# Optimization experiments

Hardware: AMD Instinct MI355X
Metric: run time of the kernel (lower is better)

Reference implementation:

```python
import jax, jax.numpy as jnp
import numpy as np

B, S, D = 2, 4096, 1024
H = 16
HD = D // H  # head_dim = 64

def setup_inputs() -> dict:
    key = jax.random.key(0)
    ks = jax.random.split(key, 9)
    sc = 1.0 / np.sqrt(D)
    return {
        "X":   jax.random.normal(ks[0], (B, S, D), dtype=jnp.float32),
        "Wq":  jax.random.normal(ks[1], (D, D), dtype=jnp.float32) * sc,
        "bq":  jax.random.normal(ks[2], (D,), dtype=jnp.float32) * 0.01,
        "Wk":  jax.random.normal(ks[3], (D, D), dtype=jnp.float32) * sc,
        "bk":  jax.random.normal(ks[4], (D,), dtype=jnp.float32) * 0.01,
        "Wv":  jax.random.normal(ks[5], (D, D), dtype=jnp.float32) * sc,
        "bv":  jax.random.normal(ks[6], (D,), dtype=jnp.float32) * 0.01,
        "Wo":  jax.random.normal(ks[7], (D, D), dtype=jnp.float32) * sc,
        "bo":  jax.random.normal(ks[8], (D,), dtype=jnp.float32) * 0.01,
    }

def reference(X, Wq, bq, Wk, bk, Wv, bv, Wo, bo):
    b, s, d = X.shape
    h, hd = H, HD
    # projections
    Q = X @ Wq + bq
    K = X @ Wk + bk
    V = X @ Wv + bv
    # [b, h, s, hd]
    Q = Q.reshape(b, s, h, hd).transpose(0, 2, 1, 3)
    K = K.reshape(b, s, h, hd).transpose(0, 2, 1, 3)
    V = V.reshape(b, s, h, hd).transpose(0, 2, 1, 3)
    scale = 1.0 / jnp.sqrt(jnp.asarray(hd, dtype=X.dtype))  # sqrt(hidden/num_heads)
    scores = jnp.einsum("bhqd,bhkd->bhqk", Q, K) * scale
    attn = jax.nn.softmax(scores, axis=-1)
    out = jnp.einsum("bhqk,bhkd->bhqd", attn, V)
    out = out.transpose(0, 2, 1, 3).reshape(b, s, d)
    return out @ Wo + bo
```

## Files before the change

kernel.cpp:

```cpp
#include <hip/hip_runtime.h>

#define Bsz 2
#define Sq  4096
#define Dm  1024
#define NH  16
#define HD  64

typedef __attribute__((ext_vector_type(8))) short short8;
typedef __attribute__((ext_vector_type(4))) float f32x4;
typedef __attribute__((ext_vector_type(2))) __fp16 fp16x2;
typedef __attribute__((ext_vector_type(4))) _Float16 half4v;

__device__ __forceinline__ unsigned short f2bf(float x) {
    unsigned int u = __float_as_uint(x);
    u += 0x7fffu + ((u >> 16) & 1u);
    return (unsigned short)(u >> 16);
}

__device__ __forceinline__ void gl2lds16(const unsigned short* g, unsigned short* l) {
    __builtin_amdgcn_global_load_lds(
        (const __attribute__((address_space(1))) unsigned int*)g,
        (__attribute__((address_space(3))) unsigned int*)l, 16, 0, 0);
}

__global__ __launch_bounds__(256) void cvt_bf16(const float4* __restrict__ in,
                                                ushort4* __restrict__ out) {
    const int i = blockIdx.x * 256 + threadIdx.x;
    const float4 v = in[i];
    ushort4 r;
    r.x = f2bf(v.x); r.y = f2bf(v.y); r.z = f2bf(v.z); r.w = f2bf(v.w);
    out[i] = r;
}

__global__ __launch_bounds__(256) void wtrans(const float* __restrict__ W,
                                              unsigned short* __restrict__ Wt) {
    __shared__ float tile[64][65];
    const int k0 = blockIdx.y * 64, n0 = blockIdx.x * 64;
    const int t = threadIdx.x;
    #pragma unroll
    for (int i = 0; i < 16; ++i) {
        const int idx = t + i * 256, r = idx >> 6, c = idx & 63;
        tile[r][c] = W[(size_t)(k0 + r) * Dm + n0 + c];
    }
    __syncthreads();
    #pragma unroll
    for (int i = 0; i < 16; ++i) {
        const int idx = t + i * 256, rr = idx >> 6, cc = idx & 63;
        Wt[(size_t)(n0 + rr) * Dm + k0 + cc] = f2bf(tile[cc][rr]);
    }
}

template <int MODE>
__global__ __launch_bounds__(256) void gemm_mfma(
    const unsigned short* __restrict__ A,
    const unsigned short* __restrict__ Bt,
    const float* __restrict__ bias,
    void* __restrict__ Cout, float oscale)
{
    __shared__ unsigned short As[128 * 32];
    __shared__ unsigned short Bs[128 * 32];

    const int bm = blockIdx.y * 128;
    const int bn = blockIdx.x * 128;
    const int t    = threadIdx.x;
    const int w    = t >> 6;
    const int lane = t & 63;
    const int quad = lane >> 4;
    const int c16  = lane & 15;
    const int wm = (w >> 1) * 64;
    const int wn = (w & 1) * 64;

    f32x4 acc[4][4];
    #pragma unroll
    for (int i = 0; i < 4; ++i)
        #pragma unroll
        for (int j = 0; j < 4; ++j)
            acc[i][j] = (f32x4){0.f, 0.f, 0.f, 0.f};

    const int srow = lane >> 2, soff = (lane & 3) * 8;
    const unsigned short* Ag0 = A  + (size_t)(bm + w * 16 + srow) * Dm + soff;
    const unsigned short* Ag1 = Ag0 + (size_t)64 * Dm;
    const unsigned short* Bg0 = Bt + (size_t)(bn + w * 16 + srow) * Dm + soff;
    const unsigned short* Bg1 = Bg0 + (size_t)64 * Dm;
    unsigned short* Al0 = As + (w * 16) * 32;
    unsigned short* Al1 = As + (64 + w * 16) * 32;
    unsigned short* Bl0 = Bs + (w * 16) * 32;
    unsigned short* Bl1 = Bs + (64 + w * 16) * 32;

    for (int k0 = 0; k0 < Dm; k0 += 32) {
        __syncthreads();
        gl2lds16(Ag0 + k0, Al0);
        gl2lds16(Ag1 + k0, Al1);
        gl2lds16(Bg0 + k0, Bl0);
        gl2lds16(Bg1 + k0, Bl1);
        __syncthreads();

        short8 af[4], bf[4];
        #pragma unroll
        for (int mt = 0; mt < 4; ++mt)
            af[mt] = *(const short8*)(As + (wm + mt * 16 + c16) * 32 + quad * 8);
        #pragma unroll
        for (int nt = 0; nt < 4; ++nt)
            bf[nt] = *(const short8*)(Bs + (wn + nt * 16 + c16) * 32 + quad * 8);
        #pragma unroll
        for (int mt = 0; mt < 4; ++mt)
            #pragma unroll
            for (int nt = 0; nt < 4; ++nt)
                acc[mt][nt] = __builtin_amdgcn_mfma_f32_16x16x32_bf16(
                    af[mt], bf[nt], acc[mt][nt], 0, 0, 0);
    }

    #pragma unroll
    for (int mt = 0; mt < 4; ++mt) {
        const int m0 = bm + wm + mt * 16 + quad * 4;
        #pragma unroll
        for (int nt = 0; nt < 4; ++nt) {
            const int n = bn + wn + nt * 16 + c16;
            const float bv = bias[n];
            if (MODE == 0) {
                float* C = (float*)Cout;
                #pragma unroll
                for (int r = 0; r < 4; ++r)
                    C[(size_t)(m0 + r) * Dm + n] = acc[mt][nt][r] + bv;
            } else if (MODE == 1) {
                unsigned short* C = (unsigned short*)Cout;
                const int h = n >> 6, d = n & 63;
                #pragma unroll
                for (int r = 0; r < 4; ++r) {
                    const int m = m0 + r;
                    const int b = m >> 12, s = m & (Sq - 1);
                    C[((size_t)(b * NH + h) * Sq + s) * HD + d] =
                        f2bf((acc[mt][nt][r] + bv) * oscale);
                }
            } else {
                unsigned short* C = (unsigned short*)Cout;
                const int h = n >> 6, d = n & 63;
                const int b = m0 >> 12, s0 = m0 & (Sq - 1);
                union { fp16x2 h2[2]; unsigned int u[2]; } pk;
                pk.h2[0] = __builtin_amdgcn_cvt_pkrtz(acc[mt][nt][0] + bv,
                                                      acc[mt][nt][1] + bv);
                pk.h2[1] = __builtin_amdgcn_cvt_pkrtz(acc[mt][nt][2] + bv,
                                                      acc[mt][nt][3] + bv);
                *(uint2*)(C + ((size_t)(b * NH + h) * HD + d) * Sq + s0) =
                    make_uint2(pk.u[0], pk.u[1]);
            }
        }
    }
}

__global__ __launch_bounds__(256, 2) void attn_mfma3(
    const unsigned short* __restrict__ Q,
    const unsigned short* __restrict__ K,
    const unsigned short* __restrict__ Vt,
    unsigned short* __restrict__ AO)
{
    __shared__ unsigned short Ks[2][64 * 72];
    __shared__ unsigned short Vs[2][64 * 72];

    const int qt = blockIdx.x;
    const int bh = blockIdx.y;
    const int b = bh >> 4, h = bh & 15;
    const int t    = threadIdx.x;
    const int w    = t >> 6;
    const int lane = t & 63;
    const int quad = lane >> 4;
    const int c16  = lane & 15;
    const size_t base = (size_t)bh * Sq * HD;

    short8 qf[4][2];
    #pragma unroll
    for (int qg = 0; qg < 4; ++qg) {
        const unsigned short* qp =
            Q + base + (size_t)(qt * 256 + w * 64 + qg * 16 + c16) * HD;
        qf[qg][0] = *(const short8*)(qp + quad * 8);
        qf[qg][1] = *(const short8*)(qp + 32 + quad * 8);
    }

    f32x4 O[4][4];
    f32x4 Lsum[4];
    #pragma unroll
    for (int qg = 0; qg < 4; ++qg) {
        Lsum[qg] = (f32x4){0.f, 0.f, 0.f, 0.f};
        #pragma unroll
        for (int g = 0; g < 4; ++g)
            O[qg][g] = (f32x4){0.f, 0.f, 0.f, 0.f};
    }
    const half4v ones = {(_Float16)1.f, (_Float16)1.f, (_Float16)1.f, (_Float16)1.f};

    const int srow = t >> 2, sc4 = (t & 3) * 8;
    const unsigned short* kg = K  + base + (size_t)srow * HD + sc4;
    const unsigned short* vg = Vt + base + (size_t)srow * Sq + sc4;
    unsigned short* ksl = &Ks[0][0] + srow * 72 + sc4;
    unsigned short* vsl = &Vs[0][0] + srow * 72 + sc4;
    const int LBUF = 64 * 72;

    int4 kr0, kr1, vr0, vr1;
    kr0 = *(const int4*)(kg);
    kr1 = *(const int4*)(kg + 32);
    vr0 = *(const int4*)(vg);
    vr1 = *(const int4*)(vg + 32);
    *(int4*)(ksl)      = kr0;
    *(int4*)(ksl + 32) = kr1;
    *(int4*)(vsl)      = vr0;
    *(int4*)(vsl + 32) = vr1;

    for (int kt = 0; kt < Sq / 64; ++kt) {
        const int cur = kt & 1;
        if (kt + 1 < Sq / 64) {
            const unsigned short* kp = kg + (size_t)(kt + 1) * 64 * HD;
            const unsigned short* vp = vg + (kt + 1) * 64;
            kr0 = *(const int4*)(kp);
            kr1 = *(const int4*)(kp + 32);
            vr0 = *(const int4*)(vp);
            vr1 = *(const int4*)(vp + 32);
        }
        __syncthreads();

        const unsigned short* ksb = &Ks[cur][0];
        const unsigned short* vsb = &Vs[cur][0];

        half4v Pfrag[4][4];
        #pragma unroll
        for (int nt = 0; nt < 4; ++nt) {
            const int krow = nt * 16 + c16;
            const short8 kf0 = *(const short8*)(ksb + krow * 72 + quad * 8);
            const short8 kf1 = *(const short8*)(ksb + krow * 72 + 32 + quad * 8);
            #pragma unroll
            for (int qg = 0; qg < 4; ++qg) {
                f32x4 z = (f32x4){0.f, 0.f, 0.f, 0.f};
                z = __builtin_amdgcn_mfma_f32_16x16x32_bf16(kf0, qf[qg][0], z, 0, 0, 0);
                z = __builtin_amdgcn_mfma_f32_16x16x32_bf16(kf1, qf[qg][1], z, 0, 0, 0);
                const float p0 = __builtin_amdgcn_exp2f(z[0]);
                const float p1 = __builtin_amdgcn_exp2f(z[1]);
                const float p2 = __builtin_amdgcn_exp2f(z[2]);
                const float p3 = __builtin_amdgcn_exp2f(z[3]);
                union { fp16x2 h2[2]; half4v h4; } pk;
                pk.h2[0] = __builtin_amdgcn_cvt_pkrtz(p0, p1);
                pk.h2[1] = __builtin_amdgcn_cvt_pkrtz(p2, p3);
                Pfrag[qg][nt] = pk.h4;
            }
        }

        #pragma unroll
        for (int kk = 0; kk < 4; ++kk) {
            #pragma unroll
            for (int g = 0; g < 4; ++g) {
                const half4v vf = *(const half4v*)
                    (vsb + (g * 16 + c16) * 72 + kk * 16 + quad * 4);
                #pragma unroll
                for (int qg = 0; qg < 4; ++qg)
                    O[qg][g] = __builtin_amdgcn_mfma_f32_16x16x16f16(
                        Pfrag[qg][kk], vf, O[qg][g], 0, 0, 0);
            }
            #pragma unroll
            for (int qg = 0; qg < 4; ++qg)
                Lsum[qg] = __builtin_amdgcn_mfma_f32_16x16x16f16(
                    Pfrag[qg][kk], ones, Lsum[qg], 0, 0, 0);
        }

        if (kt + 1 < Sq / 64) {
            const int nb = cur ^ 1;
            *(int4*)(ksl + nb * LBUF)      = kr0;
            *(int4*)(ksl + nb * LBUF + 32) = kr1;
            *(int4*)(vsl + nb * LBUF)      = vr0;
            *(int4*)(vsl + nb * LBUF + 32) = vr1;
        }
    }

    #pragma unroll
    for (int qg = 0; qg < 4; ++qg) {
        float linv[4];
        #pragma unroll
        for (int r = 0; r < 4; ++r) linv[r] = 1.f / Lsum[qg][r];
        #pragma unroll
        for (int g = 0; g < 4; ++g) {
            const int col = h * HD + g * 16 + c16;
            #pragma unroll
            for (int r = 0; r < 4; ++r) {
                const int s = qt * 256 + w * 64 + qg * 16 + quad * 4 + r;
                AO[((size_t)(b * Sq + s)) * Dm + col] = f2bf(O[qg][g][r] * linv[r]);
            }
        }
    }
}

extern "C" void kernel_launch(void* const* d_in, const int* in_sizes, int n_in,
                              void* d_out, int out_size, void* d_ws, size_t ws_size,
                              hipStream_t stream)
{
    const float* X  = (const float*)d_in[0];
    const float* Wq = (const float*)d_in[1];
    const float* bq = (const float*)d_in[2];
    const float* Wk = (const float*)d_in[3];
    const float* bk = (const float*)d_in[4];
    const float* Wv = (const float*)d_in[5];
    const float* bv = (const float*)d_in[6];
    const float* Wo = (const float*)d_in[7];
    const float* bo = (const float*)d_in[8];
    float* out = (float*)d_out;

    unsigned short* ws = (unsigned short*)d_ws;
    const size_t NX = (size_t)Bsz * Sq * Dm;
    const size_t NW = (size_t)Dm * Dm;
    unsigned short* Xb  = ws; ws += NX;
    unsigned short* Wtq = ws; ws += NW;
    unsigned short* Wtk = ws; ws += NW;
    unsigned short* Wtv = ws; ws += NW;
    unsigned short* Wto = ws; ws += NW;
    unsigned short* Qh  = ws; ws += NX;
    unsigned short* Kh  = ws; ws += NX;
    unsigned short* Vt  = ws; ws += NX;
    unsigned short* AO  = ws; ws += NX;

    cvt_bf16<<<(int)(NX / 1024), 256, 0, stream>>>((const float4*)X, (ushort4*)Xb);
    dim3 tg(16, 16);
    wtrans<<<tg, 256, 0, stream>>>(Wq, Wtq);
    wtrans<<<tg, 256, 0, stream>>>(Wk, Wtk);
    wtrans<<<tg, 256, 0, stream>>>(Wv, Wtv);
    wtrans<<<tg, 256, 0, stream>>>(Wo, Wto);

    const float SCL = 0.18033688011112042f;
    dim3 gg(Dm / 128, (Bsz * Sq) / 128);
    gemm_mfma<1><<<gg, 256, 0, stream>>>(Xb, Wtq, bq, Qh, SCL);
    gemm_mfma<1><<<gg, 256, 0, stream>>>(Xb, Wtk, bk, Kh, 1.0f);
    gemm_mfma<2><<<gg, 256, 0, stream>>>(Xb, Wtv, bv, Vt, 1.0f);

    attn_mfma3<<<dim3(Sq / 256, Bsz * NH), 256, 0, stream>>>(Qh, Kh, Vt, AO);

    gemm_mfma<0><<<gg, 256, 0, stream>>>(AO, Wto, bo, out, 1.0f);
}
```

Before: 389.2 us.

## Merge QKV GEMMs and weight transposes, halve attention query tile

Merges the four weight-transpose launches into one 3D-grid launch. The three Q/K/V projection GEMMs become a single launch over a concatenated weight buffer, with the output mode chosen per block. The attention kernel now handles 128 queries per block instead of 256, which doubles the grid to 1024 blocks, and raises the launch-bounds occupancy hint to 4 blocks. This targets launch overhead and under-filled grids, but each K/V tile loaded to shared memory is reused across fewer query rows, so K/V traffic increases.

```diff
diff --git a/kernel.cpp b/kernel.cpp
--- a/kernel.cpp
+++ b/kernel.cpp
@@ -32,9 +32,15 @@
     out[i] = r;
 }
 
-__global__ __launch_bounds__(256) void wtrans(const float* __restrict__ W,
-                                              unsigned short* __restrict__ Wt) {
+__global__ __launch_bounds__(256) void wtrans4(const float* __restrict__ Wq,
+                                               const float* __restrict__ Wk,
+                                               const float* __restrict__ Wv,
+                                               const float* __restrict__ Wo,
+                                               unsigned short* __restrict__ WtAll) {
     __shared__ float tile[64][65];
+    const int z = blockIdx.z;
+    const float* W = (z == 0) ? Wq : (z == 1) ? Wk : (z == 2) ? Wv : Wo;
+    unsigned short* Wt = WtAll + (size_t)z * Dm * Dm;
     const int k0 = blockIdx.y * 64, n0 = blockIdx.x * 64;
     const int t = threadIdx.x;
     #pragma unroll
@@ -50,32 +56,29 @@
     }
 }
 
-template <int MODE>
-__global__ __launch_bounds__(256) void gemm_mfma(
+struct GemmCtx {
+    int wm, wn, quad, c16;
+    f32x4 acc[4][4];
+};
+
+__device__ __forceinline__ void gemm_core(
     const unsigned short* __restrict__ A,
     const unsigned short* __restrict__ Bt,
-    const float* __restrict__ bias,
-    void* __restrict__ Cout, float oscale)
-{
-    __shared__ unsigned short As[128 * 32];
-    __shared__ unsigned short Bs[128 * 32];
-
-    const int bm = blockIdx.y * 128;
-    const int bn = blockIdx.x * 128;
+    int bm, int bn, unsigned short* As, unsigned short* Bs, GemmCtx& cx)
+{
     const int t    = threadIdx.x;
     const int w    = t >> 6;
     const int lane = t & 63;
-    const int quad = lane >> 4;
-    const int c16  = lane & 15;
-    const int wm = (w >> 1) * 64;
-    const int wn = (w & 1) * 64;
-
-    f32x4 acc[4][4];
+    cx.quad = lane >> 4;
+    cx.c16  = lane & 15;
+    cx.wm = (w >> 1) * 64;
+    cx.wn = (w & 1) * 64;
+
     #pragma unroll
     for (int i = 0; i < 4; ++i)
         #pragma unroll
         for (int j = 0; j < 4; ++j)
-            acc[i][j] = (f32x4){0.f, 0.f, 0.f, 0.f};
+            cx.acc[i][j] = (f32x4){0.f, 0.f, 0.f, 0.f};
 
     const int srow = lane >> 2, soff = (lane & 3) * 8;
     const unsigned short* Ag0 = A  + (size_t)(bm + w * 16 + srow) * Dm + soff;
@@ -98,57 +101,97 @@
         short8 af[4], bf[4];
         #pragma unroll
         for (int mt = 0; mt < 4; ++mt)
-            af[mt] = *(const short8*)(As + (wm + mt * 16 + c16) * 32 + quad * 8);
+            af[mt] = *(const short8*)(As + (cx.wm + mt * 16 + cx.c16) * 32 + cx.quad * 8);
         #pragma unroll
         for (int nt = 0; nt < 4; ++nt)
-            bf[nt] = *(const short8*)(Bs + (wn + nt * 16 + c16) * 32 + quad * 8);
+            bf[nt] = *(const short8*)(Bs + (cx.wn + nt * 16 + cx.c16) * 32 + cx.quad * 8);
         #pragma unroll
         for (int mt = 0; mt < 4; ++mt)
             #pragma unroll
             for (int nt = 0; nt < 4; ++nt)
-                acc[mt][nt] = __builtin_amdgcn_mfma_f32_16x16x32_bf16(
-                    af[mt], bf[nt], acc[mt][nt], 0, 0, 0);
-    }
+                cx.acc[mt][nt] = __builtin_amdgcn_mfma_f32_16x16x32_bf16(
+                    af[mt], bf[nt], cx.acc[mt][nt], 0, 0, 0);
+    }
+}
+
+__global__ __launch_bounds__(256) void gemm_qkv(
+    const unsigned short* __restrict__ A,
+    const unsigned short* __restrict__ WtAll,
+    const float* __restrict__ bq, const float* __restrict__ bk,
+    const float* __restrict__ bv,
+    unsigned short* __restrict__ Qh, unsigned short* __restrict__ Kh,
+    unsigned short* __restrict__ Vt, float qscale)
+{
+    __shared__ unsigned short As[128 * 32];
+    __shared__ unsigned short Bs[128 * 32];
+    const int bm = blockIdx.y * 128;
+    const int bn = blockIdx.x * 128;
+    GemmCtx cx;
+    gemm_core(A, WtAll, bm, bn, As, Bs, cx);
+
+    const int which = bn >> 10;
+    const float* bias = (which == 0) ? bq : (which == 1) ? bk : bv;
+    const float osc = (which == 0) ? qscale : 1.0f;
 
     #pragma unroll
     for (int mt = 0; mt < 4; ++mt) {
-        const int m0 = bm + wm + mt * 16 + quad * 4;
+        const int m0 = bm + cx.wm + mt * 16 + cx.quad * 4;
         #pragma unroll
         for (int nt = 0; nt < 4; ++nt) {
-            const int n = bn + wn + nt * 16 + c16;
-            const float bv = bias[n];
-            if (MODE == 0) {
-                float* C = (float*)Cout;
-                #pragma unroll
-                for (int r = 0; r < 4; ++r)
-                    C[(size_t)(m0 + r) * Dm + n] = acc[mt][nt][r] + bv;
-            } else if (MODE == 1) {
-                unsigned short* C = (unsigned short*)Cout;
-                const int h = n >> 6, d = n & 63;
+            const int n  = bn + cx.wn + nt * 16 + cx.c16;
+            const int nl = n & 1023;
+            const float bvv = bias[nl];
+            const int h = (nl >> 6), d = nl & 63;
+            if (which < 2) {
+                unsigned short* C = (which == 0) ? Qh : Kh;
                 #pragma unroll
                 for (int r = 0; r < 4; ++r) {
                     const int m = m0 + r;
                     const int b = m >> 12, s = m & (Sq - 1);
                     C[((size_t)(b * NH + h) * Sq + s) * HD + d] =
-                        f2bf((acc[mt][nt][r] + bv) * oscale);
+                        f2bf((cx.acc[mt][nt][r] + bvv) * osc);
                 }
             } else {
-                unsigned short* C = (unsigned short*)Cout;
-                const int h = n >> 6, d = n & 63;
                 const int b = m0 >> 12, s0 = m0 & (Sq - 1);
                 union { fp16x2 h2[2]; unsigned int u[2]; } pk;
-                pk.h2[0] = __builtin_amdgcn_cvt_pkrtz(acc[mt][nt][0] + bv,
-                                                      acc[mt][nt][1] + bv);
-                pk.h2[1] = __builtin_amdgcn_cvt_pkrtz(acc[mt][nt][2] + bv,
-                                                      acc[mt][nt][3] + bv);
-                *(uint2*)(C + ((size_t)(b * NH + h) * HD + d) * Sq + s0) =
+                pk.h2[0] = __builtin_amdgcn_cvt_pkrtz(cx.acc[mt][nt][0] + bvv,
+                                                      cx.acc[mt][nt][1] + bvv);
+                pk.h2[1] = __builtin_amdgcn_cvt_pkrtz(cx.acc[mt][nt][2] + bvv,
+                                                      cx.acc[mt][nt][3] + bvv);
+                *(uint2*)(Vt + ((size_t)(b * NH + h) * HD + d) * Sq + s0) =
                     make_uint2(pk.u[0], pk.u[1]);
             }
         }
     }
 }
 
-__global__ __launch_bounds__(256, 2) void attn_mfma3(
+__global__ __launch_bounds__(256) void gemm_o(
+    const unsigned short* __restrict__ A,
+    const unsigned short* __restrict__ Bt,
+    const float* __restrict__ bias, float* __restrict__ C)
+{
+    __shared__ unsigned short As[128 * 32];
+    __shared__ unsigned short Bs[128 * 32];
+    const int bm = blockIdx.y * 128;
+    const int bn = blockIdx.x * 128;
+    GemmCtx cx;
+    gemm_core(A, Bt, bm, bn, As, Bs, cx);
+
+    #pragma unroll
+    for (int mt = 0; mt < 4; ++mt) {
+        const int m0 = bm + cx.wm + mt * 16 + cx.quad * 4;
+        #pragma unroll
+        for (int nt = 0; nt < 4; ++nt) {
+            const int n = bn + cx.wn + nt * 16 + cx.c16;
+            const float bvv = bias[n];
+            #pragma unroll
+            for (int r = 0; r < 4; ++r)
+                C[(size_t)(m0 + r) * Dm + n] = cx.acc[mt][nt][r] + bvv;
+        }
+    }
+}
+
+__global__ __launch_bounds__(256, 4) void attn_mfma4(
     const unsigned short* __restrict__ Q,
     const unsigned short* __restrict__ K,
     const unsigned short* __restrict__ Vt,
@@ -167,19 +210,19 @@
     const int c16  = lane & 15;
     const size_t base = (size_t)bh * Sq * HD;
 
-    short8 qf[4][2];
-    #pragma unroll
-    for (int qg = 0; qg < 4; ++qg) {
+    short8 qf[2][2];
+    #pragma unroll
+    for (int qg = 0; qg < 2; ++qg) {
         const unsigned short* qp =
-            Q + base + (size_t)(qt * 256 + w * 64 + qg * 16 + c16) * HD;
+            Q + base + (size_t)(qt * 128 + w * 32 + qg * 16 + c16) * HD;
         qf[qg][0] = *(const short8*)(qp + quad * 8);
         qf[qg][1] = *(const short8*)(qp + 32 + quad * 8);
     }
 
-    f32x4 O[4][4];
-    f32x4 Lsum[4];
-    #pragma unroll
-    for (int qg = 0; qg < 4; ++qg) {
+    f32x4 O[2][4];
+    f32x4 Lsum[2];
+    #pragma unroll
+    for (int qg = 0; qg < 2; ++qg) {
         Lsum[qg] = (f32x4){0.f, 0.f, 0.f, 0.f};
         #pragma unroll
         for (int g = 0; g < 4; ++g)
@@ -219,14 +262,14 @@
         const unsigned short* ksb = &Ks[cur][0];
         const unsigned short* vsb = &Vs[cur][0];
 
-        half4v Pfrag[4][4];
+        half4v Pfrag[2][4];
         #pragma unroll
         for (int nt = 0; nt < 4; ++nt) {
             const int krow = nt * 16 + c16;
             const short8 kf0 = *(const short8*)(ksb + krow * 72 + quad * 8);
             const short8 kf1 = *(const short8*)(ksb + krow * 72 + 32 + quad * 8);
             #pragma unroll
-            for (int qg = 0; qg < 4; ++qg) {
+            for (int qg = 0; qg < 2; ++qg) {
                 f32x4 z = (f32x4){0.f, 0.f, 0.f, 0.f};
                 z = __builtin_amdgcn_mfma_f32_16x16x32_bf16(kf0, qf[qg][0], z, 0, 0, 0);
                 z = __builtin_amdgcn_mfma_f32_16x16x32_bf16(kf1, qf[qg][1], z, 0, 0, 0);
@@ -248,12 +291,12 @@
                 const half4v vf = *(const half4v*)
                     (vsb + (g * 16 + c16) * 72 + kk * 16 + quad * 4);
                 #pragma unroll
-                for (int qg = 0; qg < 4; ++qg)
+                for (int qg = 0; qg < 2; ++qg)
                     O[qg][g] = __builtin_amdgcn_mfma_f32_16x16x16f16(
                         Pfrag[qg][kk], vf, O[qg][g], 0, 0, 0);
             }
             #pragma unroll
-            for (int qg = 0; qg < 4; ++qg)
+            for (int qg = 0; qg < 2; ++qg)
                 Lsum[qg] = __builtin_amdgcn_mfma_f32_16x16x16f16(
                     Pfrag[qg][kk], ones, Lsum[qg], 0, 0, 0);
         }
@@ -268,7 +311,7 @@
     }
 
     #pragma unroll
-    for (int qg = 0; qg < 4; ++qg) {
+    for (int qg = 0; qg < 2; ++qg) {
         float linv[4];
         #pragma unroll
         for (int r = 0; r < 4; ++r) linv[r] = 1.f / Lsum[qg][r];
@@ -277,7 +320,7 @@
             const int col = h * HD + g * 16 + c16;
             #pragma unroll
             for (int r = 0; r < 4; ++r) {
-                const int s = qt * 256 + w * 64 + qg * 16 + quad * 4 + r;
+                const int s = qt * 128 + w * 32 + qg * 16 + quad * 4 + r;
                 AO[((size_t)(b * Sq + s)) * Dm + col] = f2bf(O[qg][g][r] * linv[r]);
             }
         }
@@ -302,30 +345,22 @@
     unsigned short* ws = (unsigned short*)d_ws;
     const size_t NX = (size_t)Bsz * Sq * Dm;
     const size_t NW = (size_t)Dm * Dm;
-    unsigned short* Xb  = ws; ws += NX;
-    unsigned short* Wtq = ws; ws += NW;
-    unsigned short* Wtk = ws; ws += NW;
-    unsigned short* Wtv = ws; ws += NW;
-    unsigned short* Wto = ws; ws += NW;
-    unsigned short* Qh  = ws; ws += NX;
-    unsigned short* Kh  = ws; ws += NX;
-    unsigned short* Vt  = ws; ws += NX;
-    unsigned short* AO  = ws; ws += NX;
+    unsigned short* Xb    = ws; ws += NX;
+    unsigned short* WtAll = ws; ws += 4 * NW;
+    unsigned short* Qh    = ws; ws += NX;
+    unsigned short* Kh    = ws; ws += NX;
+    unsigned short* Vt    = ws; ws += NX;
+    unsigned short* AO    = ws; ws += NX;
 
     cvt_bf16<<<(int)(NX / 1024), 256, 0, stream>>>((const float4*)X, (ushort4*)Xb);
-    dim3 tg(16, 16);
-    wtrans<<<tg, 256, 0, stream>>>(Wq, Wtq);
-    wtrans<<<tg, 256, 0, stream>>>(Wk, Wtk);
-    wtrans<<<tg, 256, 0, stream>>>(Wv, Wtv);
-    wtrans<<<tg, 256, 0, stream>>>(Wo, Wto);
+    wtrans4<<<dim3(16, 16, 4), 256, 0, stream>>>(Wq, Wk, Wv, Wo, WtAll);
 
     const float SCL = 0.18033688011112042f;
-    dim3 gg(Dm / 128, (Bsz * Sq) / 128);
-    gemm_mfma<1><<<gg, 256, 0, stream>>>(Xb, Wtq, bq, Qh, SCL);
-    gemm_mfma<1><<<gg, 256, 0, stream>>>(Xb, Wtk, bk, Kh, 1.0f);
-    gemm_mfma<2><<<gg, 256, 0, stream>>>(Xb, Wtv, bv, Vt, 1.0f);
-
-    attn_mfma3<<<dim3(Sq / 256, Bsz * NH), 256, 0, stream>>>(Qh, Kh, Vt, AO);
-
-    gemm_mfma<0><<<gg, 256, 0, stream>>>(AO, Wto, bo, out, 1.0f);
-}
+    gemm_qkv<<<dim3(3 * Dm / 128, (Bsz * Sq) / 128), 256, 0, stream>>>(
+        Xb, WtAll, bq, bk, bv, Qh, Kh, Vt, SCL);
+
+    attn_mfma4<<<dim3(Sq / 128, Bsz * NH), 256, 0, stream>>>(Qh, Kh, Vt, AO);
+
+    gemm_o<<<dim3(Dm / 128, (Bsz * Sq) / 128), 256, 0, stream>>>(
+        AO, WtAll + 3 * NW, bo, out);
+}
```

Measured after the change: 373.6 us. -4.0%, faster.
